# Kernel tuning notes

Hardware: AMD Instinct MI355X
Metric: run time of the kernel (lower is better)

## Reference

```python
import jax, jax.numpy as jnp
import numpy as np

SIGMA = 1.0


def _rbf_kernel(X, sigma):
    # pairwise squared Euclidean distances: ||xi||^2 + ||xj||^2 - 2 xi.xj
    sq = jnp.sum(X * X, axis=1)  # [n]
    d2 = sq[:, None] + sq[None, :] - 2.0 * (X @ X.T)
    d2 = jnp.maximum(d2, 0.0)
    return jnp.exp(-d2 / (2.0 * sigma ** 2))


def _center(K):
    # Kc = H @ K @ H with H = I - 11^T/n, done in O(n^2):
    # Kc = K - row_mean - col_mean + grand_mean
    row_mean = jnp.mean(K, axis=1, keepdims=True)   # [n,1]
    col_mean = jnp.mean(K, axis=0, keepdims=True)   # [1,n]
    grand = jnp.mean(K)
    return K - row_mean - col_mean + grand


def setup_inputs() -> dict:
    key = jax.random.key(0)
    k1, k2 = jax.random.split(key)
    X = jax.random.normal(k1, (8192, 512), dtype=jnp.float32)
    Y = jax.random.normal(k2, (8192, 512), dtype=jnp.float32)
    return {"X": X, "Y": Y}


def reference(X, Y):
    n = X.shape[0]
    K = _rbf_kernel(X, SIGMA)
    L = _rbf_kernel(Y, SIGMA)
    Kc = _center(K)
    Lc = _center(L)
    # trace(Kc @ Lc) == sum(Kc * Lc^T) == sum(Kc * Lc) since Lc symmetric
    hsic_value = jnp.sum(Kc * Lc) / (n - 1) ** 2
    return hsic_value
```

## Files before the change

### kernel.cpp

```cpp
#include <hip/hip_runtime.h>
#include <hip/hip_bf16.h>

#define N 8192
#define D 512

typedef __attribute__((ext_vector_type(4))) float f32x4;
typedef __attribute__((ext_vector_type(2))) long i64x2;

#define WAITVM(n) asm volatile("s_waitcnt vmcnt(" #n ")" ::: "memory")
#define WAITLGKM asm volatile("s_waitcnt lgkmcnt(0)" ::: "memory")
#define BAR __builtin_amdgcn_s_barrier()

__device__ __forceinline__ void g2l16(const void* g, void* l) {
  __builtin_amdgcn_global_load_lds(
      (const __attribute__((address_space(1))) void*)g,
      (__attribute__((address_space(3))) void*)l, 16, 0, 0);
}

__global__ __launch_bounds__(128) void prep_kernel(
    const float* __restrict__ X, const float* __restrict__ Y,
    unsigned char* __restrict__ Xb, unsigned char* __restrict__ Yb,
    float* __restrict__ sqX, float* __restrict__ sqY) {
  const int b = blockIdx.x;
  const int row = b & (N - 1);
  const float* src = (b < N) ? X : Y;
  unsigned char* dst = (b < N) ? Xb : Yb;
  float* sq = (b < N) ? sqX : sqY;
  const int t = threadIdx.x;
  float4 v = reinterpret_cast<const float4*>(src + (size_t)row * D)[t];
  unsigned p = __builtin_amdgcn_cvt_pk_fp8_f32(v.x, v.y, 0, false);
  p = __builtin_amdgcn_cvt_pk_fp8_f32(v.z, v.w, p, true);
  float f0 = __builtin_amdgcn_cvt_f32_fp8(p, 0);
  float f1 = __builtin_amdgcn_cvt_f32_fp8(p, 1);
  float f2 = __builtin_amdgcn_cvt_f32_fp8(p, 2);
  float f3 = __builtin_amdgcn_cvt_f32_fp8(p, 3);
  float s = f0 * f0 + f1 * f1 + f2 * f2 + f3 * f3;
  const int g = t >> 4;
  const int kl = (t & 15) * 4;
  const int dest = g * 64 + ((kl & 31) >> 3) * 16 + (kl >> 5) * 8 + (kl & 7);
  *reinterpret_cast<unsigned*>(dst + (size_t)row * D + dest) = p;
  #pragma unroll
  for (int msk = 1; msk < 64; msk <<= 1) s += __shfl_xor(s, msk);
  __shared__ float red[2];
  if ((t & 63) == 0) red[t >> 6] = s;
  __syncthreads();
  if (t == 0) sq[row] = red[0] + red[1];
}

__global__ __launch_bounds__(256, 4) void hsic_main(
    const unsigned char* __restrict__ Xb, const unsigned char* __restrict__ Yb,
    const float* __restrict__ sqX, const float* __restrict__ sqY,
    float* __restrict__ rowK, float* __restrict__ rowL,
    float* __restrict__ sums) {
  __shared__ __align__(16) unsigned char sbuf[2][2][128 * 64];

  const int bid = (blockIdx.x & 7) * 260 + (blockIdx.x >> 3);
  int ti = (int)((129.0f - sqrtf(16641.0f - 8.0f * (float)bid)) * 0.5f);
  while (ti > 0 && (ti * (129 - ti)) / 2 > bid) --ti;
  while (((ti + 1) * (128 - ti)) / 2 <= bid) ++ti;
  const int tj = ti + (bid - (ti * (129 - ti)) / 2);
  const bool diag = (ti == tj);

  const int ib = ti * 128, jb = tj * 128;
  const int t = threadIdx.x;
  const int lane = t & 63, wave = t >> 6;
  const int wr = wave >> 1, wc = wave & 1;
  const int fr = lane & 15, fq = lane >> 4;

  f32x4 acc[4][4];
  #pragma unroll
  for (int m = 0; m < 4; ++m)
    #pragma unroll
    for (int n = 0; n < 4; ++n) acc[m][n] = (f32x4)0.f;

  const unsigned char* s0 = Xb + (size_t)ib * D;
  const unsigned char* s1 = Xb + (size_t)jb * D;
  const unsigned char* s2 = Yb + (size_t)ib * D;
  const unsigned char* s3 = Yb + (size_t)jb * D;

  const int srow = t >> 2;
  const int swcb = ((t & 3) * 16) ^ (((t >> 3) & 3) << 4);
  const int lo16 = t * 16;

  auto stage = [&](int kt, int p, bool isY) {
    const unsigned char* si = isY ? s2 : s0;
    const unsigned char* sj = isY ? s3 : s1;
    #pragma unroll
    for (int q = 0; q < 2; ++q) {
      const size_t goff = (size_t)(q * 64 + srow) * D + kt * 64 + swcb;
      const int lo = q * 4096 + lo16;
      g2l16(si + goff, &sbuf[p][0][lo]);
      g2l16(sj + goff, &sbuf[p][1][lo]);
    }
  };

  const int fcol = (fq * 16) ^ (((fr >> 1) & 3) << 4);

  i64x2 a[4], b[4];
  auto frags = [&](int p) {
    const unsigned char* si = sbuf[p][0];
    const unsigned char* sj = sbuf[p][1];
    #pragma unroll
    for (int m = 0; m < 4; ++m)
      a[m] = *(const i64x2*)&si[(wr * 64 + m * 16 + fr) * 64 + fcol];
    #pragma unroll
    for (int n = 0; n < 4; ++n)
      b[n] = *(const i64x2*)&sj[(wc * 64 + n * 16 + fr) * 64 + fcol];
  };
  auto mma = [&]() {
    __builtin_amdgcn_s_setprio(1);
    #pragma unroll
    for (int m = 0; m < 4; ++m)
      #pragma unroll
      for (int n = 0; n < 4; ++n) {
        acc[m][n] = __builtin_amdgcn_mfma_f32_16x16x32_fp8_fp8(a[m][0], b[n][0], acc[m][n], 0, 0, 0);
        acc[m][n] = __builtin_amdgcn_mfma_f32_16x16x32_fp8_fp8(a[m][1], b[n][1], acc[m][n], 0, 0, 0);
      }
    __builtin_amdgcn_s_setprio(0);
  };

  stage(0, 0, false); stage(1, 1, false);
  #pragma unroll 1
  for (int kt = 0; kt < 6; ++kt) {
    WAITVM(4); BAR;
    frags(kt & 1);
    WAITLGKM; BAR;
    stage(kt + 2, kt & 1, false);
    mma();
  }
  WAITVM(4); BAR; frags(0); WAITLGKM; BAR;
  stage(0, 0, true);
  mma();
  WAITVM(4); BAR; frags(1); WAITLGKM; BAR;
  stage(1, 1, true);
  mma();

  unsigned kp[16];
  {
    float sxj[4];
    #pragma unroll
    for (int n = 0; n < 4; ++n) sxj[n] = sqX[jb + wc * 64 + n * 16 + fr];
    float ckK[4] = {0.f, 0.f, 0.f, 0.f};
    #pragma unroll
    for (int m = 0; m < 4; ++m) {
      #pragma unroll
      for (int r = 0; r < 4; ++r) {
        const int i = ib + wr * 64 + m * 16 + fq * 4 + r;
        const float sxi = sqX[i];
        float Kv[4];
        float rk = 0.f;
        #pragma unroll
        for (int n = 0; n < 4; ++n) {
          float dK = fmaxf(sxi + sxj[n] - 2.f * acc[m][n][r], 0.f);
          Kv[n] = __expf(-0.5f * dK);
          rk += Kv[n];
          ckK[n] += Kv[n];
        }
        unsigned pk = __builtin_amdgcn_cvt_pk_fp8_f32(Kv[0], Kv[1], 0, false);
        kp[m * 4 + r] = __builtin_amdgcn_cvt_pk_fp8_f32(Kv[2], Kv[3], pk, true);
        #pragma unroll
        for (int msk = 1; msk < 16; msk <<= 1) rk += __shfl_xor(rk, msk);
        if (fr == 0) atomicAdd(&rowK[i], rk);
      }
    }
    if (!diag) {
      #pragma unroll
      for (int n = 0; n < 4; ++n) {
        float a2 = ckK[n];
        a2 += __shfl_xor(a2, 16); a2 += __shfl_xor(a2, 32);
        if (fq == 0) atomicAdd(&rowK[jb + wc * 64 + n * 16 + fr], a2);
      }
    }
  }

  #pragma unroll
  for (int m = 0; m < 4; ++m)
    #pragma unroll
    for (int n = 0; n < 4; ++n) acc[m][n] = (f32x4)0.f;

  #pragma unroll 1
  for (int kt = 0; kt < 6; ++kt) {
    WAITVM(4); BAR;
    frags(kt & 1);
    WAITLGKM; BAR;
    stage(kt + 2, kt & 1, true);
    mma();
  }
  WAITVM(4); BAR; frags(0); WAITLGKM; mma();
  WAITVM(0); BAR; frags(1); WAITLGKM; mma();

  float sxj[4];
  #pragma unroll
  for (int n = 0; n < 4; ++n) sxj[n] = sqY[jb + wc * 64 + n * 16 + fr];
  float kl = 0.f;
  float ckL[4] = {0.f, 0.f, 0.f, 0.f};
  #pragma unroll
  for (int m = 0; m < 4; ++m) {
    #pragma unroll
    for (int r = 0; r < 4; ++r) {
      const int i = ib + wr * 64 + m * 16 + fq * 4 + r;
      const float syi = sqY[i];
      const unsigned pk = kp[m * 4 + r];
      const float Kvv[4] = {__builtin_amdgcn_cvt_f32_fp8(pk, 0),
                            __builtin_amdgcn_cvt_f32_fp8(pk, 1),
                            __builtin_amdgcn_cvt_f32_fp8(pk, 2),
                            __builtin_amdgcn_cvt_f32_fp8(pk, 3)};
      float rl = 0.f;
      #pragma unroll
      for (int n = 0; n < 4; ++n) {
        float dL = fmaxf(syi + sxj[n] - 2.f * acc[m][n][r], 0.f);
        float Lv = __expf(-0.5f * dL);
        kl += Kvv[n] * Lv;
        rl += Lv;
        ckL[n] += Lv;
      }
      #pragma unroll
      for (int msk = 1; msk < 16; msk <<= 1) rl += __shfl_xor(rl, msk);
      if (fr == 0) atomicAdd(&rowL[i], rl);
    }
  }
  if (!diag) {
    #pragma unroll
    for (int n = 0; n < 4; ++n) {
      float b2 = ckL[n];
      b2 += __shfl_xor(b2, 16); b2 += __shfl_xor(b2, 32);
      if (fq == 0) atomicAdd(&rowL[jb + wc * 64 + n * 16 + fr], b2);
    }
    kl *= 2.f;
  }
  #pragma unroll
  for (int msk = 1; msk < 64; msk <<= 1) kl += __shfl_xor(kl, msk);
  __shared__ float klred[4];
  if (lane == 0) klred[wave] = kl;
  __syncthreads();
  if (t == 0) atomicAdd(sums, klred[0] + klred[1] + klred[2] + klred[3]);
}

__global__ __launch_bounds__(256) void finalize_kernel(
    const float* __restrict__ rowK, const float* __restrict__ rowL,
    const float* __restrict__ sums, float* __restrict__ out) {
  const int t = threadIdx.x;
  float dp = 0.f, sk = 0.f, sl = 0.f;
  for (int i = t; i < N; i += 256) {
    float a = rowK[i], b = rowL[i];
    dp += a * b; sk += a; sl += b;
  }
  #pragma unroll
  for (int msk = 1; msk < 64; msk <<= 1) {
    dp += __shfl_xor(dp, msk);
    sk += __shfl_xor(sk, msk);
    sl += __shfl_xor(sl, msk);
  }
  __shared__ float r[3][4];
  const int wave = t >> 6, lane = t & 63;
  if (lane == 0) { r[0][wave] = dp; r[1][wave] = sk; r[2][wave] = sl; }
  __syncthreads();
  if (t == 0) {
    float DP = r[0][0] + r[0][1] + r[0][2] + r[0][3];
    float SK = r[1][0] + r[1][1] + r[1][2] + r[1][3];
    float SL = r[2][0] + r[2][1] + r[2][2] + r[2][3];
    const float n = (float)N;
    float raw = sums[0] - (2.f / n) * DP + (SK / n) * (SL / n);
    out[0] = raw / ((n - 1.f) * (n - 1.f));
  }
}

extern "C" void kernel_launch(void* const* d_in, const int* in_sizes, int n_in,
                              void* d_out, int out_size, void* d_ws, size_t ws_size,
                              hipStream_t stream) {
  const float* X = (const float*)d_in[0];
  const float* Y = (const float*)d_in[1];
  char* ws = (char*)d_ws;
  unsigned char* Xb = (unsigned char*)ws;
  unsigned char* Yb = (unsigned char*)(ws + (size_t)N * D);
  float* sqX = (float*)(ws + (size_t)2 * N * D);
  float* sqY = sqX + N;
  float* rowK = sqY + N;
  float* rowL = rowK + N;
  float* sums = rowL + N;

  (void)hipMemsetAsync(rowK, 0, (size_t)(2 * N + 16) * sizeof(float), stream);
  prep_kernel<<<2 * N, 128, 0, stream>>>(X, Y, Xb, Yb, sqX, sqY);
  const int ntiles = (N / 128) * (N / 128 + 1) / 2;
  hsic_main<<<ntiles, 256, 0, stream>>>(Xb, Yb, sqX, sqY, rowK, rowL, sums);
  finalize_kernel<<<1, 256, 0, stream>>>(rowK, rowL, sums, (float*)d_out);
}
```

Before: 174.8 us.

## Compute X and Y Gram tiles concurrently with 8 waves per block

Doubles the block to 512 threads so four waves compute the X Gram tile while four others compute the Y Gram tile concurrently, instead of one set of waves doing both in sequence. All four operand tiles are staged together each k-step, and K values are exchanged through LDS in fp32 rather than packed to fp8 in registers. The X waves write K and the Y waves read it after a barrier. This raises LDS use to 64KB per block and asks for 4 blocks of 512 threads per CU, which limits occupancy and increases register pressure. The Y waves also sit idle while the X waves run their epilogue.

```diff
diff --git a/kernel.cpp b/kernel.cpp
--- a/kernel.cpp
+++ b/kernel.cpp
@@ -47,12 +47,13 @@
   if (t == 0) sq[row] = red[0] + red[1];
 }
 
-__global__ __launch_bounds__(256, 4) void hsic_main(
+__global__ __launch_bounds__(512, 4) void hsic_main(
     const unsigned char* __restrict__ Xb, const unsigned char* __restrict__ Yb,
     const float* __restrict__ sqX, const float* __restrict__ sqY,
     float* __restrict__ rowK, float* __restrict__ rowL,
     float* __restrict__ sums) {
-  __shared__ __align__(16) unsigned char sbuf[2][2][128 * 64];
+  __shared__ __align__(16) unsigned char sbuf[2][4][128 * 64];
+  __shared__ float klred[4];
 
   const int bid = (blockIdx.x & 7) * 260 + (blockIdx.x >> 3);
   int ti = (int)((129.0f - sqrtf(16641.0f - 8.0f * (float)bid)) * 0.5f);
@@ -64,7 +65,9 @@
   const int ib = ti * 128, jb = tj * 128;
   const int t = threadIdx.x;
   const int lane = t & 63, wave = t >> 6;
-  const int wr = wave >> 1, wc = wave & 1;
+  const bool isY = wave >= 4;
+  const int wid = wave & 3;
+  const int wr = wid >> 1, wc = wid & 1;
   const int fr = lane & 15, fq = lane >> 4;
 
   f32x4 acc[4][4];
@@ -80,26 +83,23 @@
 
   const int srow = t >> 2;
   const int swcb = ((t & 3) * 16) ^ (((t >> 3) & 3) << 4);
+  const size_t gbase = (size_t)srow * D + swcb;
   const int lo16 = t * 16;
 
-  auto stage = [&](int kt, int p, bool isY) {
-    const unsigned char* si = isY ? s2 : s0;
-    const unsigned char* sj = isY ? s3 : s1;
-    #pragma unroll
-    for (int q = 0; q < 2; ++q) {
-      const size_t goff = (size_t)(q * 64 + srow) * D + kt * 64 + swcb;
-      const int lo = q * 4096 + lo16;
-      g2l16(si + goff, &sbuf[p][0][lo]);
-      g2l16(sj + goff, &sbuf[p][1][lo]);
-    }
+  auto stage = [&](int kt, int p) {
+    const size_t go = gbase + kt * 64;
+    g2l16(s0 + go, &sbuf[p][0][lo16]);
+    g2l16(s1 + go, &sbuf[p][1][lo16]);
+    g2l16(s2 + go, &sbuf[p][2][lo16]);
+    g2l16(s3 + go, &sbuf[p][3][lo16]);
   };
 
   const int fcol = (fq * 16) ^ (((fr >> 1) & 3) << 4);
 
   i64x2 a[4], b[4];
   auto frags = [&](int p) {
-    const unsigned char* si = sbuf[p][0];
-    const unsigned char* sj = sbuf[p][1];
+    const unsigned char* si = sbuf[p][isY ? 2 : 0];
+    const unsigned char* sj = sbuf[p][isY ? 3 : 1];
     #pragma unroll
     for (int m = 0; m < 4; ++m)
       a[m] = *(const i64x2*)&si[(wr * 64 + m * 16 + fr) * 64 + fcol];
@@ -119,45 +119,43 @@
     __builtin_amdgcn_s_setprio(0);
   };
 
-  stage(0, 0, false); stage(1, 1, false);
+  stage(0, 0); stage(1, 1);
   #pragma unroll 1
   for (int kt = 0; kt < 6; ++kt) {
-    WAITVM(4); BAR;
+    WAITVM(4);
+    BAR;
     frags(kt & 1);
-    WAITLGKM; BAR;
-    stage(kt + 2, kt & 1, false);
+    WAITLGKM;
+    BAR;
+    stage(kt + 2, kt & 1);
     mma();
   }
-  WAITVM(4); BAR; frags(0); WAITLGKM; BAR;
-  stage(0, 0, true);
-  mma();
-  WAITVM(4); BAR; frags(1); WAITLGKM; BAR;
-  stage(1, 1, true);
-  mma();
-
-  unsigned kp[16];
-  {
-    float sxj[4];
-    #pragma unroll
-    for (int n = 0; n < 4; ++n) sxj[n] = sqX[jb + wc * 64 + n * 16 + fr];
-    float ckK[4] = {0.f, 0.f, 0.f, 0.f};
+  WAITVM(4); BAR; frags(0); WAITLGKM; mma();
+  WAITVM(0); BAR; frags(1); WAITLGKM; mma();
+
+  BAR;
+  float* kvs = (float*)sbuf;
+  const float* sqP = isY ? sqY : sqX;
+  float sqj[4];
+  #pragma unroll
+  for (int n = 0; n < 4; ++n) sqj[n] = sqP[jb + wc * 64 + n * 16 + fr];
+
+  if (!isY) {
+    float ck[4] = {0.f, 0.f, 0.f, 0.f};
     #pragma unroll
     for (int m = 0; m < 4; ++m) {
       #pragma unroll
       for (int r = 0; r < 4; ++r) {
         const int i = ib + wr * 64 + m * 16 + fq * 4 + r;
         const float sxi = sqX[i];
-        float Kv[4];
         float rk = 0.f;
         #pragma unroll
         for (int n = 0; n < 4; ++n) {
-          float dK = fmaxf(sxi + sxj[n] - 2.f * acc[m][n][r], 0.f);
-          Kv[n] = __expf(-0.5f * dK);
-          rk += Kv[n];
-          ckK[n] += Kv[n];
+          float dK = fmaxf(sxi + sqj[n] - 2.f * acc[m][n][r], 0.f);
+          float Kv = __expf(-0.5f * dK);
+          rk += Kv; ck[n] += Kv;
+          kvs[wid * 4096 + ((m * 4 + r) * 4 + n) * 64 + lane] = Kv;
         }
-        unsigned pk = __builtin_amdgcn_cvt_pk_fp8_f32(Kv[0], Kv[1], 0, false);
-        kp[m * 4 + r] = __builtin_amdgcn_cvt_pk_fp8_f32(Kv[2], Kv[3], pk, true);
         #pragma unroll
         for (int msk = 1; msk < 16; msk <<= 1) rk += __shfl_xor(rk, msk);
         if (fr == 0) atomicAdd(&rowK[i], rk);
@@ -166,74 +164,52 @@
     if (!diag) {
       #pragma unroll
       for (int n = 0; n < 4; ++n) {
-        float a2 = ckK[n];
+        float a2 = ck[n];
         a2 += __shfl_xor(a2, 16); a2 += __shfl_xor(a2, 32);
         if (fq == 0) atomicAdd(&rowK[jb + wc * 64 + n * 16 + fr], a2);
       }
     }
   }
-
-  #pragma unroll
-  for (int m = 0; m < 4; ++m)
-    #pragma unroll
-    for (int n = 0; n < 4; ++n) acc[m][n] = (f32x4)0.f;
-
-  #pragma unroll 1
-  for (int kt = 0; kt < 6; ++kt) {
-    WAITVM(4); BAR;
-    frags(kt & 1);
-    WAITLGKM; BAR;
-    stage(kt + 2, kt & 1, true);
-    mma();
-  }
-  WAITVM(4); BAR; frags(0); WAITLGKM; mma();
-  WAITVM(0); BAR; frags(1); WAITLGKM; mma();
-
-  float sxj[4];
-  #pragma unroll
-  for (int n = 0; n < 4; ++n) sxj[n] = sqY[jb + wc * 64 + n * 16 + fr];
-  float kl = 0.f;
-  float ckL[4] = {0.f, 0.f, 0.f, 0.f};
-  #pragma unroll
-  for (int m = 0; m < 4; ++m) {
-    #pragma unroll
-    for (int r = 0; r < 4; ++r) {
-      const int i = ib + wr * 64 + m * 16 + fq * 4 + r;
-      const float syi = sqY[i];
-      const unsigned pk = kp[m * 4 + r];
-      const float Kvv[4] = {__builtin_amdgcn_cvt_f32_fp8(pk, 0),
-                            __builtin_amdgcn_cvt_f32_fp8(pk, 1),
-                            __builtin_amdgcn_cvt_f32_fp8(pk, 2),
-                            __builtin_amdgcn_cvt_f32_fp8(pk, 3)};
-      float rl = 0.f;
+  BAR;
+  if (isY) {
+    float kl = 0.f;
+    float ck[4] = {0.f, 0.f, 0.f, 0.f};
+    #pragma unroll
+    for (int m = 0; m < 4; ++m) {
+      #pragma unroll
+      for (int r = 0; r < 4; ++r) {
+        const int i = ib + wr * 64 + m * 16 + fq * 4 + r;
+        const float syi = sqY[i];
+        float rl = 0.f;
+        #pragma unroll
+        for (int n = 0; n < 4; ++n) {
+          float dL = fmaxf(syi + sqj[n] - 2.f * acc[m][n][r], 0.f);
+          float Lv = __expf(-0.5f * dL);
+          float Kv = kvs[wid * 4096 + ((m * 4 + r) * 4 + n) * 64 + lane];
+          kl += Kv * Lv;
+          rl += Lv; ck[n] += Lv;
+        }
+        #pragma unroll
+        for (int msk = 1; msk < 16; msk <<= 1) rl += __shfl_xor(rl, msk);
+        if (fr == 0) atomicAdd(&rowL[i], rl);
+      }
+    }
+    if (!diag) {
       #pragma unroll
       for (int n = 0; n < 4; ++n) {
-        float dL = fmaxf(syi + sxj[n] - 2.f * acc[m][n][r], 0.f);
-        float Lv = __expf(-0.5f * dL);
-        kl += Kvv[n] * Lv;
-        rl += Lv;
-        ckL[n] += Lv;
-      }
-      #pragma unroll
-      for (int msk = 1; msk < 16; msk <<= 1) rl += __shfl_xor(rl, msk);
-      if (fr == 0) atomicAdd(&rowL[i], rl);
-    }
-  }
-  if (!diag) {
-    #pragma unroll
-    for (int n = 0; n < 4; ++n) {
-      float b2 = ckL[n];
-      b2 += __shfl_xor(b2, 16); b2 += __shfl_xor(b2, 32);
-      if (fq == 0) atomicAdd(&rowL[jb + wc * 64 + n * 16 + fr], b2);
-    }
-    kl *= 2.f;
-  }
-  #pragma unroll
-  for (int msk = 1; msk < 64; msk <<= 1) kl += __shfl_xor(kl, msk);
-  __shared__ float klred[4];
-  if (lane == 0) klred[wave] = kl;
+        float b2 = ck[n];
+        b2 += __shfl_xor(b2, 16); b2 += __shfl_xor(b2, 32);
+        if (fq == 0) atomicAdd(&rowL[jb + wc * 64 + n * 16 + fr], b2);
+      }
+      kl *= 2.f;
+    }
+    #pragma unroll
+    for (int msk = 1; msk < 64; msk <<= 1) kl += __shfl_xor(kl, msk);
+    if (lane == 0) klred[wid] = kl;
+  }
   __syncthreads();
-  if (t == 0) atomicAdd(sums, klred[0] + klred[1] + klred[2] + klred[3]);
+  if (t == 0)
+    atomicAdd(sums, klred[0] + klred[1] + klred[2] + klred[3]);
 }
 
 __global__ __launch_bounds__(256) void finalize_kernel(
@@ -282,6 +258,6 @@
   (void)hipMemsetAsync(rowK, 0, (size_t)(2 * N + 16) * sizeof(float), stream);
   prep_kernel<<<2 * N, 128, 0, stream>>>(X, Y, Xb, Yb, sqX, sqY);
   const int ntiles = (N / 128) * (N / 128 + 1) / 2;
-  hsic_main<<<ntiles, 256, 0, stream>>>(Xb, Yb, sqX, sqY, rowK, rowL, sums);
+  hsic_main<<<ntiles, 512, 0, stream>>>(Xb, Yb, sqX, sqY, rowK, rowL, sums);
   finalize_kernel<<<1, 256, 0, stream>>>(rowK, rowL, sums, (float*)d_out);
 }
```

After: 217.7 us. 24.5% more time.
